# Kernel tuning notes

Hardware: AMD Instinct MI355X
Metric: run time of the kernel (lower is better)

Reference implementation:

```python
import jax, jax.numpy as jnp
import numpy as np

NUM_HEADS = 12
HEAD_DIM = 32  # all_head_size(384) / num_heads(12)


def setup_inputs() -> dict:
    key = jax.random.key(0)
    ks = jax.random.split(key, 8)
    B, Sq, Sk, Din, AH = 1, 4096, 4096, 768, 384
    scale = 1.0 / np.sqrt(Din)
    return {
        "hidden_states": jax.random.normal(ks[0], (B, Sq, Din), jnp.float32),
        "encoder_hidden_states": jax.random.normal(ks[1], (B, Sk, Din), jnp.float32),
        "encoder_attention_mask": jnp.zeros((B, 1, 1, Sk), jnp.float32),
        "Wq": jax.random.normal(ks[2], (Din, AH), jnp.float32) * scale,
        "bq": jnp.zeros((AH,), jnp.float32),
        "Wk": jax.random.normal(ks[3], (Din, AH), jnp.float32) * scale,
        "bk": jnp.zeros((AH,), jnp.float32),
        "Wv": jax.random.normal(ks[4], (Din, AH), jnp.float32) * scale,
        "bv": jnp.zeros((AH,), jnp.float32),
    }


def _split_heads(x):
    # [B, S, H*D] -> [B, H, S, D]
    B, S, _ = x.shape
    return x.reshape(B, S, NUM_HEADS, HEAD_DIM).transpose(0, 2, 1, 3)


def reference(hidden_states, encoder_hidden_states, encoder_attention_mask,
              Wq, bq, Wk, bk, Wv, bv):
    q = _split_heads(hidden_states @ Wq + bq)            # [B,H,Sq,D]
    k = _split_heads(encoder_hidden_states @ Wk + bk)    # [B,H,Sk,D]
    v = _split_heads(encoder_hidden_states @ Wv + bv)    # [B,H,Sk,D]

    scores = jnp.einsum('bhqd,bhkd->bhqk', q, k) / np.sqrt(HEAD_DIM)
    scores = scores + encoder_attention_mask              # additive mask, broadcast
    probs = jax.nn.softmax(scores, axis=-1)               # dropout is identity (eval)

    ctx = jnp.einsum('bhqk,bhkd->bhqd', probs, v)         # [B,H,Sq,D]
    B, H, Sq, D = ctx.shape
    return ctx.transpose(0, 2, 1, 3).reshape(B, Sq, H * D)  # [B,Sq,all_head_size]
```

## Files before the change

kernel.cpp:

```cpp
#include <hip/hip_runtime.h>
#include <hip/hip_bf16.h>

#define SQ 4096
#define SKK 4096
#define DIN 768
#define AHS 384
#define NHEAD 12
#define HD 32

typedef __attribute__((ext_vector_type(8))) short bf16x8;
typedef __attribute__((ext_vector_type(4))) float f32x4;
typedef __attribute__((ext_vector_type(4))) unsigned int u32x4;

#define LOG2E 1.4426950408889634f
#define QSCALE 0.25503486168652855f

__device__ __forceinline__ unsigned short bf16_rn(float x){
  unsigned int u = __float_as_uint(x);
  unsigned int r = u + 0x7fffu + ((u>>16)&1u);
  return (unsigned short)(r>>16);
}
__device__ __forceinline__ float bf16_f(unsigned short h){
  return __uint_as_float(((unsigned int)h)<<16);
}
__device__ __forceinline__ float fexp2(float x){
#if __has_builtin(__builtin_amdgcn_exp2f)
  return __builtin_amdgcn_exp2f(x);
#else
  float r; asm("v_exp_f32 %0, %1" : "=v"(r) : "v"(x)); return r;
#endif
}

__global__ void prep_wt_kernel(const float* __restrict__ Wq, const float* __restrict__ Wk,
                               const float* __restrict__ Wv, const float* __restrict__ mask,
                               unsigned short* __restrict__ Wthi, unsigned short* __restrict__ Wtlo,
                               unsigned short* __restrict__ EMB){
  int idx = blockIdx.x*256 + threadIdx.x;
  if (idx < SKK) EMB[idx] = bf16_rn(__expf(mask[idx]));
  const int per = DIN*AHS;
  if (idx >= 3*per) return;
  int mat = idx/per, rem = idx - mat*per;
  int k = rem/AHS, n = rem - k*AHS;
  const float* W = (mat==0)?Wq:((mat==1)?Wk:Wv);
  float v = W[k*AHS+n];
  unsigned short hh = bf16_rn(v);
  unsigned short ll = bf16_rn(v - bf16_f(hh));
  Wthi[mat*per + n*DIN + k] = hh;
  Wtlo[mat*per + n*DIN + k] = ll;
}

__global__ __launch_bounds__(512,4) void proj2_kernel(
    const float* __restrict__ Xh, const float* __restrict__ Xe,
    const unsigned short* __restrict__ Wthi, const unsigned short* __restrict__ Wtlo,
    const float* __restrict__ bq, const float* __restrict__ bk, const float* __restrict__ bv,
    const unsigned short* __restrict__ EMB,
    unsigned short* __restrict__ Qhi, unsigned short* __restrict__ Qlo,
    unsigned short* __restrict__ Khi, unsigned short* __restrict__ Klo,
    unsigned short* __restrict__ Vt)
{
  const int z = blockIdx.z;
  const float* A = (z==0) ? Xh : Xe;
  const unsigned short* Bh = Wthi + (size_t)z*(DIN*AHS);
  const unsigned short* Bl = Wtlo + (size_t)z*(DIN*AHS);
  const float* bias = (z==0) ? bq : ((z==1) ? bk : bv);

  const int m0 = blockIdx.x*128;
  const int n0 = blockIdx.y*128;
  const int tid = threadIdx.x;
  const int w = tid>>6, lane = tid&63;
  const int lm = lane&15, g = lane>>4;
  const int wm = w>>1, wn = w&1;

  __shared__ __align__(16) unsigned short SH[32768];

  const int srow = tid>>2, scol = (tid&3)*8;
  const float* pA = A + (size_t)(m0 + srow)*DIN + scol;
  const size_t gb = (size_t)(n0 + srow)*DIN + scol;
  const int sidx = srow*32 + ((((tid&3) ^ ((srow>>1)&3)))<<3);

  f32x4 xa0, xa1; u32x4 rb, rlb;
  auto sload = [&](int kk){
    xa0 = *(const f32x4*)(pA + kk);
    xa1 = *(const f32x4*)(pA + kk + 4);
    rb  = *(const u32x4*)(Bh + gb + kk);
    if (z != 2) rlb = *(const u32x4*)(Bl + gb + kk);
  };
  auto swrite = [&](int b){
    float xx[8] = {xa0[0],xa0[1],xa0[2],xa0[3],xa1[0],xa1[1],xa1[2],xa1[3]};
    unsigned int hw[4];
    #pragma unroll
    for (int p=0;p<4;++p)
      asm("v_cvt_pk_bf16_f32 %0, %1, %2" : "=v"(hw[p]) : "v"(xx[2*p]), "v"(xx[2*p+1]));
    u32x4 ra = {hw[0],hw[1],hw[2],hw[3]};
    *(u32x4*)&SH[b*16384 + 0*4096 + sidx] = ra;
    *(u32x4*)&SH[b*16384 + 2*4096 + sidx] = rb;
    if (z != 2){
      unsigned int lw[4];
      #pragma unroll
      for (int p=0;p<4;++p){
        float h0 = __uint_as_float(hw[p]<<16);
        float h1 = __uint_as_float(hw[p] & 0xffff0000u);
        float l0 = xx[2*p] - h0, l1 = xx[2*p+1] - h1;
        asm("v_cvt_pk_bf16_f32 %0, %1, %2" : "=v"(lw[p]) : "v"(l0), "v"(l1));
      }
      u32x4 rla = {lw[0],lw[1],lw[2],lw[3]};
      *(u32x4*)&SH[b*16384 + 1*4096 + sidx] = rla;
      *(u32x4*)&SH[b*16384 + 3*4096 + sidx] = rlb;
    }
  };

  f32x4 acc[2][4];
  #pragma unroll
  for (int mi=0;mi<2;++mi)
    #pragma unroll
    for (int ni=0;ni<4;++ni) acc[mi][ni] = (f32x4){0.f,0.f,0.f,0.f};

  auto fidx = [&](int row)->int{ return row*32 + ((g ^ ((row>>1)&3))<<3); };

  sload(0); swrite(0); __syncthreads();
  int cur = 0;

  const int NKS = DIN/32;
  for (int t=0; t<NKS; ++t){
    if (t+1 < NKS) sload((t+1)*32);

    const unsigned short* AhL = &SH[cur*16384 + 0*4096];
    const unsigned short* AlL = &SH[cur*16384 + 1*4096];
    const unsigned short* BhL = &SH[cur*16384 + 2*4096];
    const unsigned short* BlL = &SH[cur*16384 + 3*4096];

    bf16x8 a0h = *(const bf16x8*)&AhL[fidx(wm*32 + lm)];
    bf16x8 a1h = *(const bf16x8*)&AhL[fidx(wm*32 + 16 + lm)];
    bf16x8 a0l, a1l;
    if (z != 2){
      a0l = *(const bf16x8*)&AlL[fidx(wm*32 + lm)];
      a1l = *(const bf16x8*)&AlL[fidx(wm*32 + 16 + lm)];
    }
    __builtin_amdgcn_s_setprio(1);
    #pragma unroll
    for (int ni=0; ni<4; ++ni){
      bf16x8 bh = *(const bf16x8*)&BhL[fidx(wn*64 + ni*16 + lm)];
      acc[0][ni] = __builtin_amdgcn_mfma_f32_16x16x32_bf16(a0h, bh, acc[0][ni], 0,0,0);
      acc[1][ni] = __builtin_amdgcn_mfma_f32_16x16x32_bf16(a1h, bh, acc[1][ni], 0,0,0);
      if (z != 2){
        bf16x8 bl = *(const bf16x8*)&BlL[fidx(wn*64 + ni*16 + lm)];
        acc[0][ni] = __builtin_amdgcn_mfma_f32_16x16x32_bf16(a0h, bl, acc[0][ni], 0,0,0);
        acc[1][ni] = __builtin_amdgcn_mfma_f32_16x16x32_bf16(a1h, bl, acc[1][ni], 0,0,0);
        acc[0][ni] = __builtin_amdgcn_mfma_f32_16x16x32_bf16(a0l, bh, acc[0][ni], 0,0,0);
        acc[1][ni] = __builtin_amdgcn_mfma_f32_16x16x32_bf16(a1l, bh, acc[1][ni], 0,0,0);
      }
    }
    __builtin_amdgcn_s_setprio(0);

    if (t+1 < NKS) swrite(cur^1);
    __syncthreads();
    cur ^= 1;
  }

  if (z != 2){
    #pragma unroll
    for (int ni=0; ni<4; ++ni){
      int col = n0 + wn*64 + ni*16 + lm;
      float bcol = bias[col];
      int hq = col>>5, d = col&31;
      #pragma unroll
      for (int mi=0; mi<2; ++mi){
        #pragma unroll
        for (int r=0; r<4; ++r){
          int row = m0 + wm*32 + mi*16 + g*4 + r;
          float v = acc[mi][ni][r] + bcol;
          if (z==0) v *= QSCALE;
          unsigned short hh = bf16_rn(v);
          unsigned short ll = bf16_rn(v - bf16_f(hh));
          size_t p = (z==0) ? ((size_t)hq*SQ + row)*HD + d
                            : ((size_t)hq*SKK + row)*HD + d;
          if (z==0){ Qhi[p]=hh; Qlo[p]=ll; } else { Khi[p]=hh; Klo[p]=ll; }
        }
      }
    }
  } else {
    #pragma unroll
    for (int ni=0; ni<4; ++ni){
      int lcol = wn*64 + ni*16 + lm;
      float bcol = bias[n0 + lcol];
      #pragma unroll
      for (int mi=0; mi<2; ++mi){
        #pragma unroll
        for (int r=0; r<4; ++r){
          int lrow = wm*32 + mi*16 + g*4 + r;
          float emf = bf16_f(EMB[m0 + lrow]);
          SH[lcol*128 + (lrow ^ ((lcol&7)<<3))] = bf16_rn((acc[mi][ni][r] + bcol) * emf);
        }
      }
    }
    __syncthreads();
    #pragma unroll
    for (int p=0; p<4; ++p){
      int c = tid>>2, rc = (tid&3)*8 + p*32;
      bf16x8 vv = *(const bf16x8*)&SH[c*128 + (rc ^ ((c&7)<<3))];
      *(bf16x8*)(Vt + (size_t)(n0 + c)*SKK + m0 + rc) = vv;
    }
  }
}

__global__ __launch_bounds__(256) void attn_kernel(
    const unsigned short* __restrict__ Qhi, const unsigned short* __restrict__ Qlo,
    const unsigned short* __restrict__ Khi, const unsigned short* __restrict__ Klo,
    const unsigned short* __restrict__ Vt, const unsigned short* __restrict__ EMB,
    float* __restrict__ opart, float* __restrict__ lpart,
    int nkt, int direct)
{
  const int qt = blockIdx.x, h = blockIdx.y, sp = blockIdx.z;
  const int tid = threadIdx.x;
  const int w = tid>>6, lane = tid&63;
  const int lm = lane&15, g = lane>>4;
  const int qrow = qt*64 + w*16 + lm;
  const int kbeg = sp*nkt*64;

  __shared__ unsigned short KhL[2][2048];
  __shared__ unsigned short KlL[2][2048];
  __shared__ unsigned short VL [2][2048];

  const int krow_s = tid>>2, kc = tid&3;
  const int ksw = ((krow_s>>1)&1) ^ (((krow_s>>3)&1)<<1);
  const int kds = krow_s*32 + ((kc ^ ksw)<<3);
  const int vrow_s = tid>>3;
  const int vds = vrow_s*64 + (((tid&7) ^ (vrow_s&7))<<3);

  const unsigned short* pKh = Khi + (size_t)h*SKK*HD + (size_t)(kbeg+krow_s)*HD + kc*8;
  const unsigned short* pKl = Klo + (size_t)h*SKK*HD + (size_t)(kbeg+krow_s)*HD + kc*8;
  const unsigned short* pV  = Vt + (size_t)(h*HD + vrow_s)*SKK + kbeg + (tid&7)*8;
  const unsigned short* pEM = EMB + kbeg + g*8;

  const int krs = ((lm>>2)<<3) + (lm&3);
  const int rsw = ((krs>>1)&1) ^ (((krs>>3)&1)<<1);
  const int kread0 = krs*32 + ((g ^ rsw)<<3);

  int vr[4];
  vr[0] = (lm*64      + g*8)      ^ ((lm&7)<<3);
  vr[1] = (lm*64      + 32 + g*8) ^ ((lm&7)<<3);
  vr[2] = ((lm+16)*64 + g*8)      ^ ((lm&7)<<3);
  vr[3] = ((lm+16)*64 + 32 + g*8) ^ ((lm&7)<<3);

  bf16x8 qh = *(const bf16x8*)(Qhi + ((size_t)h*SQ + qrow)*HD + g*8);
  bf16x8 ql = *(const bf16x8*)(Qlo + ((size_t)h*SQ + qrow)*HD + g*8);

  f32x4 o0 = {0.f,0.f,0.f,0.f}, o1 = {0.f,0.f,0.f,0.f};
  f32x4 lacc = {0.f,0.f,0.f,0.f};

  u32x4 sa = *(const u32x4*)pKh;
  u32x4 sb = *(const u32x4*)pKl;
  u32x4 sc = *(const u32x4*)pV;
  *(u32x4*)(&KhL[0][kds]) = sa;
  *(u32x4*)(&KlL[0][kds]) = sb;
  *(u32x4*)(&VL [0][vds]) = sc;
  __syncthreads();

  #pragma unroll 2
  for (int t=0; t<nkt; ++t){
    const int cur = t&1;

    if (t+1 < nkt){
      pKh += 64*HD; pKl += 64*HD; pV += 64;
      sa = *(const u32x4*)pKh;
      sb = *(const u32x4*)pKl;
      sc = *(const u32x4*)pV;
    }

    bf16x8 em0 = *(const bf16x8*)(pEM);
    bf16x8 em1 = *(const bf16x8*)(pEM + 32);
    pEM += 64;

    unsigned int wds[8];
    #pragma unroll
    for (int ks=0; ks<4; ++ks){
      const int kidx = kread0 + (ks&1)*128 + (ks>>1)*1024;
      bf16x8 kh = *(const bf16x8*)(&KhL[cur][kidx]);
      bf16x8 kl = *(const bf16x8*)(&KlL[cur][kidx]);
      f32x4 a = {0.f,0.f,0.f,0.f};
      __builtin_amdgcn_s_setprio(1);
      a = __builtin_amdgcn_mfma_f32_16x16x32_bf16(kh, qh, a, 0,0,0);
      a = __builtin_amdgcn_mfma_f32_16x16x32_bf16(kh, ql, a, 0,0,0);
      a = __builtin_amdgcn_mfma_f32_16x16x32_bf16(kl, qh, a, 0,0,0);
      __builtin_amdgcn_s_setprio(0);
      float p0 = fexp2(a[0]);
      float p1 = fexp2(a[1]);
      float p2 = fexp2(a[2]);
      float p3 = fexp2(a[3]);
      asm("v_cvt_pk_bf16_f32 %0, %1, %2" : "=v"(wds[ks*2])   : "v"(p0), "v"(p1));
      asm("v_cvt_pk_bf16_f32 %0, %1, %2" : "=v"(wds[ks*2+1]) : "v"(p2), "v"(p3));
    }
    u32x4 w0v = {wds[0], wds[1], wds[2], wds[3]};
    u32x4 w1v = {wds[4], wds[5], wds[6], wds[7]};
    bf16x8 pa0 = __builtin_bit_cast(bf16x8, w0v);
    bf16x8 pa1 = __builtin_bit_cast(bf16x8, w1v);

    bf16x8 v00 = *(const bf16x8*)(&VL[cur][vr[0]]);
    bf16x8 v01 = *(const bf16x8*)(&VL[cur][vr[1]]);
    bf16x8 v10 = *(const bf16x8*)(&VL[cur][vr[2]]);
    bf16x8 v11 = *(const bf16x8*)(&VL[cur][vr[3]]);
    __builtin_amdgcn_s_setprio(1);
    o0   = __builtin_amdgcn_mfma_f32_16x16x32_bf16(pa0, v00, o0,   0,0,0);
    o1   = __builtin_amdgcn_mfma_f32_16x16x32_bf16(pa0, v10, o1,   0,0,0);
    lacc = __builtin_amdgcn_mfma_f32_16x16x32_bf16(pa0, em0, lacc, 0,0,0);
    o0   = __builtin_amdgcn_mfma_f32_16x16x32_bf16(pa1, v01, o0,   0,0,0);
    o1   = __builtin_amdgcn_mfma_f32_16x16x32_bf16(pa1, v11, o1,   0,0,0);
    lacc = __builtin_amdgcn_mfma_f32_16x16x32_bf16(pa1, em1, lacc, 0,0,0);
    __builtin_amdgcn_s_setprio(0);

    if (t+1 < nkt){
      *(u32x4*)(&KhL[cur^1][kds]) = sa;
      *(u32x4*)(&KlL[cur^1][kds]) = sb;
      *(u32x4*)(&VL [cur^1][vds]) = sc;
    }
    __syncthreads();
  }

  if (direct){
    #pragma unroll
    for (int r=0;r<4;++r){
      float inv = 1.0f / lacc[r];
      int row = qt*64 + w*16 + g*4 + r;
      opart[(size_t)row*AHS + h*HD + lm]      = o0[r]*inv;
      opart[(size_t)row*AHS + h*HD + 16 + lm] = o1[r]*inv;
    }
  } else {
    #pragma unroll
    for (int r=0;r<4;++r){
      int row = qt*64 + w*16 + g*4 + r;
      opart[((size_t)sp*SQ + row)*AHS + h*HD + lm]      = o0[r];
      opart[((size_t)sp*SQ + row)*AHS + h*HD + 16 + lm] = o1[r];
    }
    if (lm == 0){
      #pragma unroll
      for (int r=0;r<4;++r){
        int row = qt*64 + w*16 + g*4 + r;
        lpart[((size_t)sp*NHEAD + h)*SQ + row] = lacc[r];
      }
    }
  }
}

__global__ void merge_kernel(const float* __restrict__ opart,
                             const float* __restrict__ lpart,
                             float* __restrict__ out, int S){
  int idx = blockIdx.x*256 + threadIdx.x;
  if (idx >= SQ*AHS) return;
  int row = idx/AHS, c = idx - row*AHS;
  int h = c >> 5;
  float num = 0.f, den = 0.f;
  for (int s=0; s<S; ++s){
    num += opart[((size_t)s*SQ + row)*AHS + c];
    den += lpart[((size_t)s*NHEAD + h)*SQ + row];
  }
  out[idx] = num/den;
}

extern "C" void kernel_launch(void* const* d_in, const int* in_sizes, int n_in,
                              void* d_out, int out_size, void* d_ws, size_t ws_size,
                              hipStream_t stream) {
  const float* Xh   = (const float*)d_in[0];
  const float* Xe   = (const float*)d_in[1];
  const float* mask = (const float*)d_in[2];
  const float* Wq   = (const float*)d_in[3];
  const float* bq   = (const float*)d_in[4];
  const float* Wk   = (const float*)d_in[5];
  const float* bk   = (const float*)d_in[6];
  const float* Wv   = (const float*)d_in[7];
  const float* bv   = (const float*)d_in[8];
  float* out = (float*)d_out;

  char* ws = (char*)d_ws;
  auto al256 = [](size_t b)->size_t{ return (b + 255) & ~(size_t)255; };
  size_t off = 0;
  auto alloc = [&](size_t bytes)->void*{ void* p = ws + off; off += al256(bytes); return p; };

  unsigned short* Wthi = (unsigned short*)alloc((size_t)3*DIN*AHS*2);
  unsigned short* Wtlo = (unsigned short*)alloc((size_t)3*DIN*AHS*2);
  unsigned short* EMB  = (unsigned short*)alloc((size_t)SKK*2);
  unsigned short* Qhi  = (unsigned short*)alloc((size_t)NHEAD*SQ*HD*2);
  unsigned short* Qlo  = (unsigned short*)alloc((size_t)NHEAD*SQ*HD*2);
  unsigned short* Khi  = (unsigned short*)alloc((size_t)NHEAD*SKK*HD*2);
  unsigned short* Klo  = (unsigned short*)alloc((size_t)NHEAD*SKK*HD*2);
  unsigned short* Vt   = (unsigned short*)alloc((size_t)AHS*SKK*2);
  const size_t base_end = off;

  const size_t OB = al256((size_t)SQ*AHS*4);
  const size_t MB = al256((size_t)NHEAD*SQ*4);

  auto fits = [&](int S)->bool{
    return base_end + (size_t)S*OB + (size_t)S*MB + 8192 <= ws_size;
  };

  int S = 1, direct = 0;
  if      (fits(4)) S = 4;
  else if (fits(2)) S = 2;
  else if (fits(1)) S = 1;
  else { S = 1; direct = 1; }

  char* ureg = ws + base_end;
  float *opart, *lpart;
  if (!direct){
    opart = (float*)(ureg);
    lpart = (float*)(ureg + (size_t)S*OB);
  } else {
    opart = out; lpart = (float*)ws;
  }

  {
    int tot = 3*DIN*AHS;
    prep_wt_kernel<<<(tot+255)/256, 256, 0, stream>>>(Wq, Wk, Wv, mask, Wthi, Wtlo, EMB);
  }
  {
    dim3 grid(SQ/128, AHS/128, 3);
    proj2_kernel<<<grid, 512, 0, stream>>>(Xh, Xe, Wthi, Wtlo,
                                           bq, bk, bv, EMB, Qhi, Qlo, Khi, Klo, Vt);
  }
  {
    dim3 grid(SQ/64, NHEAD, S);
    int nkt = (SKK/64)/S;
    attn_kernel<<<grid, 256, 0, stream>>>(Qhi, Qlo, Khi, Klo, Vt, EMB,
                                          opart, lpart, nkt, direct);
  }
  if (!direct){
    int n = SQ*AHS;
    merge_kernel<<<(n+255)/256, 256, 0, stream>>>(opart, lpart, out, S);
  }
}
```

Baseline: 117.5 us.

## Use direct global-to-LDS loads in attention and shrink projection tiles

The attention kernel now stages K and V tiles with global_load_lds (direct global-to-LDS DMA), issued for the next tile before compute, instead of loading through registers and writing LDS afterwards. The projection kernel drops to 64x64 tiles with 256 threads and reads the B (weight) fragments straight from global memory, so only A goes through LDS. This aims to cut register pressure and LDS write traffic and to give the projection more blocks. The risks are that async LDS loads may not be properly awaited before the barrier, and that the uncached per-lane global weight reads may add latency.

```diff
diff --git a/kernel.cpp b/kernel.cpp
--- a/kernel.cpp
+++ b/kernel.cpp
@@ -14,6 +14,10 @@
 
 #define LOG2E 1.4426950408889634f
 #define QSCALE 0.25503486168652855f
+
+#define GLD16(gp, lp) __builtin_amdgcn_global_load_lds( \
+    (const __attribute__((address_space(1))) void*)(gp), \
+    (__attribute__((address_space(3))) void*)(lp), 16, 0, 0)
 
 __device__ __forceinline__ unsigned short bf16_rn(float x){
   unsigned int u = __float_as_uint(x);
@@ -49,7 +53,7 @@
   Wtlo[mat*per + n*DIN + k] = ll;
 }
 
-__global__ __launch_bounds__(512,4) void proj2_kernel(
+__global__ __launch_bounds__(256,4) void proj3_kernel(
     const float* __restrict__ Xh, const float* __restrict__ Xe,
     const unsigned short* __restrict__ Wthi, const unsigned short* __restrict__ Wtlo,
     const float* __restrict__ bq, const float* __restrict__ bk, const float* __restrict__ bv,
@@ -64,103 +68,106 @@
   const unsigned short* Bl = Wtlo + (size_t)z*(DIN*AHS);
   const float* bias = (z==0) ? bq : ((z==1) ? bk : bv);
 
-  const int m0 = blockIdx.x*128;
-  const int n0 = blockIdx.y*128;
+  const int m0 = blockIdx.x*64;
+  const int n0 = blockIdx.y*64;
   const int tid = threadIdx.x;
   const int w = tid>>6, lane = tid&63;
   const int lm = lane&15, g = lane>>4;
   const int wm = w>>1, wn = w&1;
 
-  __shared__ __align__(16) unsigned short SH[32768];
-
-  const int srow = tid>>2, scol = (tid&3)*8;
-  const float* pA = A + (size_t)(m0 + srow)*DIN + scol;
-  const size_t gb = (size_t)(n0 + srow)*DIN + scol;
-  const int sidx = srow*32 + ((((tid&3) ^ ((srow>>1)&3)))<<3);
-
-  f32x4 xa0, xa1; u32x4 rb, rlb;
+  __shared__ __align__(16) unsigned short SA[2][2][2048];
+
+  const int srow = tid>>2, scn = tid&3;
+  const int sidx = srow*32 + ((scn ^ ((srow>>1)&3))<<3);
+  const float* pA = A + (size_t)(m0 + srow)*DIN + scn*8;
+
+  const unsigned short* pb0h = Bh + (size_t)(n0 + wn*32 + lm)*DIN + g*8;
+  const unsigned short* pb1h = pb0h + 16*DIN;
+  const unsigned short* pb0l = Bl + (size_t)(n0 + wn*32 + lm)*DIN + g*8;
+  const unsigned short* pb1l = pb0l + 16*DIN;
+
+  f32x4 xa0, xa1;
   auto sload = [&](int kk){
     xa0 = *(const f32x4*)(pA + kk);
     xa1 = *(const f32x4*)(pA + kk + 4);
-    rb  = *(const u32x4*)(Bh + gb + kk);
-    if (z != 2) rlb = *(const u32x4*)(Bl + gb + kk);
   };
   auto swrite = [&](int b){
-    float xx[8] = {xa0[0],xa0[1],xa0[2],xa0[3],xa1[0],xa1[1],xa1[2],xa1[3]};
     unsigned int hw[4];
-    #pragma unroll
-    for (int p=0;p<4;++p)
-      asm("v_cvt_pk_bf16_f32 %0, %1, %2" : "=v"(hw[p]) : "v"(xx[2*p]), "v"(xx[2*p+1]));
+    asm("v_cvt_pk_bf16_f32 %0, %1, %2" : "=v"(hw[0]) : "v"(xa0[0]), "v"(xa0[1]));
+    asm("v_cvt_pk_bf16_f32 %0, %1, %2" : "=v"(hw[1]) : "v"(xa0[2]), "v"(xa0[3]));
+    asm("v_cvt_pk_bf16_f32 %0, %1, %2" : "=v"(hw[2]) : "v"(xa1[0]), "v"(xa1[1]));
+    asm("v_cvt_pk_bf16_f32 %0, %1, %2" : "=v"(hw[3]) : "v"(xa1[2]), "v"(xa1[3]));
     u32x4 ra = {hw[0],hw[1],hw[2],hw[3]};
-    *(u32x4*)&SH[b*16384 + 0*4096 + sidx] = ra;
-    *(u32x4*)&SH[b*16384 + 2*4096 + sidx] = rb;
+    *(u32x4*)&SA[b][0][sidx] = ra;
     if (z != 2){
+      float xs[8] = {xa0[0],xa0[1],xa0[2],xa0[3],xa1[0],xa1[1],xa1[2],xa1[3]};
       unsigned int lw[4];
       #pragma unroll
       for (int p=0;p<4;++p){
         float h0 = __uint_as_float(hw[p]<<16);
         float h1 = __uint_as_float(hw[p] & 0xffff0000u);
-        float l0 = xx[2*p] - h0, l1 = xx[2*p+1] - h1;
+        float l0 = xs[2*p] - h0, l1 = xs[2*p+1] - h1;
         asm("v_cvt_pk_bf16_f32 %0, %1, %2" : "=v"(lw[p]) : "v"(l0), "v"(l1));
       }
       u32x4 rla = {lw[0],lw[1],lw[2],lw[3]};
-      *(u32x4*)&SH[b*16384 + 1*4096 + sidx] = rla;
-      *(u32x4*)&SH[b*16384 + 3*4096 + sidx] = rlb;
+      *(u32x4*)&SA[b][1][sidx] = rla;
     }
   };
 
-  f32x4 acc[2][4];
+  f32x4 acc[2][2];
   #pragma unroll
   for (int mi=0;mi<2;++mi)
     #pragma unroll
-    for (int ni=0;ni<4;++ni) acc[mi][ni] = (f32x4){0.f,0.f,0.f,0.f};
+    for (int ni=0;ni<2;++ni) acc[mi][ni] = (f32x4){0.f,0.f,0.f,0.f};
 
   auto fidx = [&](int row)->int{ return row*32 + ((g ^ ((row>>1)&3))<<3); };
 
   sload(0); swrite(0); __syncthreads();
-  int cur = 0;
 
   const int NKS = DIN/32;
+  #pragma unroll
   for (int t=0; t<NKS; ++t){
+    const int cur = t&1;
     if (t+1 < NKS) sload((t+1)*32);
 
-    const unsigned short* AhL = &SH[cur*16384 + 0*4096];
-    const unsigned short* AlL = &SH[cur*16384 + 1*4096];
-    const unsigned short* BhL = &SH[cur*16384 + 2*4096];
-    const unsigned short* BlL = &SH[cur*16384 + 3*4096];
-
-    bf16x8 a0h = *(const bf16x8*)&AhL[fidx(wm*32 + lm)];
-    bf16x8 a1h = *(const bf16x8*)&AhL[fidx(wm*32 + 16 + lm)];
-    bf16x8 a0l, a1l;
+    bf16x8 a0h = *(const bf16x8*)&SA[cur][0][fidx(wm*32 + lm)];
+    bf16x8 a1h = *(const bf16x8*)&SA[cur][0][fidx(wm*32 + 16 + lm)];
+    const int kko = t*32;
+    bf16x8 b0h = *(const bf16x8*)(pb0h + kko);
+    bf16x8 b1h = *(const bf16x8*)(pb1h + kko);
+
+    __builtin_amdgcn_s_setprio(1);
+    acc[0][0] = __builtin_amdgcn_mfma_f32_16x16x32_bf16(a0h, b0h, acc[0][0], 0,0,0);
+    acc[1][0] = __builtin_amdgcn_mfma_f32_16x16x32_bf16(a1h, b0h, acc[1][0], 0,0,0);
+    acc[0][1] = __builtin_amdgcn_mfma_f32_16x16x32_bf16(a0h, b1h, acc[0][1], 0,0,0);
+    acc[1][1] = __builtin_amdgcn_mfma_f32_16x16x32_bf16(a1h, b1h, acc[1][1], 0,0,0);
+    __builtin_amdgcn_s_setprio(0);
+
     if (z != 2){
-      a0l = *(const bf16x8*)&AlL[fidx(wm*32 + lm)];
-      a1l = *(const bf16x8*)&AlL[fidx(wm*32 + 16 + lm)];
-    }
-    __builtin_amdgcn_s_setprio(1);
-    #pragma unroll
-    for (int ni=0; ni<4; ++ni){
-      bf16x8 bh = *(const bf16x8*)&BhL[fidx(wn*64 + ni*16 + lm)];
-      acc[0][ni] = __builtin_amdgcn_mfma_f32_16x16x32_bf16(a0h, bh, acc[0][ni], 0,0,0);
-      acc[1][ni] = __builtin_amdgcn_mfma_f32_16x16x32_bf16(a1h, bh, acc[1][ni], 0,0,0);
-      if (z != 2){
-        bf16x8 bl = *(const bf16x8*)&BlL[fidx(wn*64 + ni*16 + lm)];
-        acc[0][ni] = __builtin_amdgcn_mfma_f32_16x16x32_bf16(a0h, bl, acc[0][ni], 0,0,0);
-        acc[1][ni] = __builtin_amdgcn_mfma_f32_16x16x32_bf16(a1h, bl, acc[1][ni], 0,0,0);
-        acc[0][ni] = __builtin_amdgcn_mfma_f32_16x16x32_bf16(a0l, bh, acc[0][ni], 0,0,0);
-        acc[1][ni] = __builtin_amdgcn_mfma_f32_16x16x32_bf16(a1l, bh, acc[1][ni], 0,0,0);
-      }
-    }
-    __builtin_amdgcn_s_setprio(0);
+      bf16x8 a0l = *(const bf16x8*)&SA[cur][1][fidx(wm*32 + lm)];
+      bf16x8 a1l = *(const bf16x8*)&SA[cur][1][fidx(wm*32 + 16 + lm)];
+      bf16x8 b0l = *(const bf16x8*)(pb0l + kko);
+      bf16x8 b1l = *(const bf16x8*)(pb1l + kko);
+      __builtin_amdgcn_s_setprio(1);
+      acc[0][0] = __builtin_amdgcn_mfma_f32_16x16x32_bf16(a0h, b0l, acc[0][0], 0,0,0);
+      acc[1][0] = __builtin_amdgcn_mfma_f32_16x16x32_bf16(a1h, b0l, acc[1][0], 0,0,0);
+      acc[0][1] = __builtin_amdgcn_mfma_f32_16x16x32_bf16(a0h, b1l, acc[0][1], 0,0,0);
+      acc[1][1] = __builtin_amdgcn_mfma_f32_16x16x32_bf16(a1h, b1l, acc[1][1], 0,0,0);
+      acc[0][0] = __builtin_amdgcn_mfma_f32_16x16x32_bf16(a0l, b0h, acc[0][0], 0,0,0);
+      acc[1][0] = __builtin_amdgcn_mfma_f32_16x16x32_bf16(a1l, b0h, acc[1][0], 0,0,0);
+      acc[0][1] = __builtin_amdgcn_mfma_f32_16x16x32_bf16(a0l, b1h, acc[0][1], 0,0,0);
+      acc[1][1] = __builtin_amdgcn_mfma_f32_16x16x32_bf16(a1l, b1h, acc[1][1], 0,0,0);
+      __builtin_amdgcn_s_setprio(0);
+    }
 
     if (t+1 < NKS) swrite(cur^1);
     __syncthreads();
-    cur ^= 1;
   }
 
   if (z != 2){
     #pragma unroll
-    for (int ni=0; ni<4; ++ni){
-      int col = n0 + wn*64 + ni*16 + lm;
+    for (int ni=0; ni<2; ++ni){
+      int col = n0 + wn*32 + ni*16 + lm;
       float bcol = bias[col];
       int hq = col>>5, d = col&31;
       #pragma unroll
@@ -179,9 +186,10 @@
       }
     }
   } else {
-    #pragma unroll
-    for (int ni=0; ni<4; ++ni){
-      int lcol = wn*64 + ni*16 + lm;
+    unsigned short* SH2 = &SA[0][0][0];
+    #pragma unroll
+    for (int ni=0; ni<2; ++ni){
+      int lcol = wn*32 + ni*16 + lm;
       float bcol = bias[n0 + lcol];
       #pragma unroll
       for (int mi=0; mi<2; ++mi){
@@ -189,15 +197,15 @@
         for (int r=0; r<4; ++r){
           int lrow = wm*32 + mi*16 + g*4 + r;
           float emf = bf16_f(EMB[m0 + lrow]);
-          SH[lcol*128 + (lrow ^ ((lcol&7)<<3))] = bf16_rn((acc[mi][ni][r] + bcol) * emf);
+          SH2[lcol*64 + (lrow ^ ((lcol&7)<<3))] = bf16_rn((acc[mi][ni][r] + bcol) * emf);
         }
       }
     }
     __syncthreads();
     #pragma unroll
-    for (int p=0; p<4; ++p){
+    for (int p=0; p<2; ++p){
       int c = tid>>2, rc = (tid&3)*8 + p*32;
-      bf16x8 vv = *(const bf16x8*)&SH[c*128 + (rc ^ ((c&7)<<3))];
+      bf16x8 vv = *(const bf16x8*)&SH2[c*64 + (rc ^ ((c&7)<<3))];
       *(bf16x8*)(Vt + (size_t)(n0 + c)*SKK + m0 + rc) = vv;
     }
   }
@@ -221,15 +229,15 @@
   __shared__ unsigned short KlL[2][2048];
   __shared__ unsigned short VL [2][2048];
 
-  const int krow_s = tid>>2, kc = tid&3;
-  const int ksw = ((krow_s>>1)&1) ^ (((krow_s>>3)&1)<<1);
-  const int kds = krow_s*32 + ((kc ^ ksw)<<3);
-  const int vrow_s = tid>>3;
-  const int vds = vrow_s*64 + (((tid&7) ^ (vrow_s&7))<<3);
-
-  const unsigned short* pKh = Khi + (size_t)h*SKK*HD + (size_t)(kbeg+krow_s)*HD + kc*8;
-  const unsigned short* pKl = Klo + (size_t)h*SKK*HD + (size_t)(kbeg+krow_s)*HD + kc*8;
-  const unsigned short* pV  = Vt + (size_t)(h*HD + vrow_s)*SKK + kbeg + (tid&7)*8;
+  const int krow_l = 16*w + (lane>>2);
+  const int ksw_l = ((krow_l>>1)&1) ^ (((krow_l>>3)&1)<<1);
+  const unsigned short* gKh = Khi + (size_t)h*SKK*HD
+                            + (size_t)(kbeg + krow_l)*HD + (((lane&3)^ksw_l)<<3);
+  const unsigned short* gKl = Klo + (size_t)h*SKK*HD
+                            + (size_t)(kbeg + krow_l)*HD + (((lane&3)^ksw_l)<<3);
+  const int vrow_l = 8*w + (lane>>3);
+  const unsigned short* gV = Vt + (size_t)(h*HD + vrow_l)*SKK + kbeg
+                           + (((lane&7)^(lane>>3))<<3);
   const unsigned short* pEM = EMB + kbeg + g*8;
 
   const int krs = ((lm>>2)<<3) + (lm&3);
@@ -248,12 +256,9 @@
   f32x4 o0 = {0.f,0.f,0.f,0.f}, o1 = {0.f,0.f,0.f,0.f};
   f32x4 lacc = {0.f,0.f,0.f,0.f};
 
-  u32x4 sa = *(const u32x4*)pKh;
-  u32x4 sb = *(const u32x4*)pKl;
-  u32x4 sc = *(const u32x4*)pV;
-  *(u32x4*)(&KhL[0][kds]) = sa;
-  *(u32x4*)(&KlL[0][kds]) = sb;
-  *(u32x4*)(&VL [0][vds]) = sc;
+  GLD16(gKh, &KhL[0][w*512]);
+  GLD16(gKl, &KlL[0][w*512]);
+  GLD16(gV,  &VL [0][w*512]);
   __syncthreads();
 
   #pragma unroll 2
@@ -261,10 +266,10 @@
     const int cur = t&1;
 
     if (t+1 < nkt){
-      pKh += 64*HD; pKl += 64*HD; pV += 64;
-      sa = *(const u32x4*)pKh;
-      sb = *(const u32x4*)pKl;
-      sc = *(const u32x4*)pV;
+      gKh += 64*HD; gKl += 64*HD; gV += 64;
+      GLD16(gKh, &KhL[cur^1][w*512]);
+      GLD16(gKl, &KlL[cur^1][w*512]);
+      GLD16(gV,  &VL [cur^1][w*512]);
     }
 
     bf16x8 em0 = *(const bf16x8*)(pEM);
@@ -308,11 +313,6 @@
     lacc = __builtin_amdgcn_mfma_f32_16x16x32_bf16(pa1, em1, lacc, 0,0,0);
     __builtin_amdgcn_s_setprio(0);
 
-    if (t+1 < nkt){
-      *(u32x4*)(&KhL[cur^1][kds]) = sa;
-      *(u32x4*)(&KlL[cur^1][kds]) = sb;
-      *(u32x4*)(&VL [cur^1][vds]) = sc;
-    }
     __syncthreads();
   }
 
@@ -412,8 +412,8 @@
     prep_wt_kernel<<<(tot+255)/256, 256, 0, stream>>>(Wq, Wk, Wv, mask, Wthi, Wtlo, EMB);
   }
   {
-    dim3 grid(SQ/128, AHS/128, 3);
-    proj2_kernel<<<grid, 512, 0, stream>>>(Xh, Xe, Wthi, Wtlo,
+    dim3 grid(SQ/64, AHS/64, 3);
+    proj3_kernel<<<grid, 256, 0, stream>>>(Xh, Xe, Wthi, Wtlo,
                                            bq, bk, bv, EMB, Qhi, Qlo, Khi, Klo, Vt);
   }
   {
```

New measurement: 138.9 us. 18.2% more time.
